# Optimization experiments

Hardware: AMD Instinct MI355X
Metric: run time of the kernel (lower is better)

Reference implementation:

```python
import jax, jax.numpy as jnp
import numpy as np

H, DM, DK, DV, DFF = 8, 512, 64, 64, 2048
B, S = 8, 1024
EPS = 1e-5


def layernorm_global(x):
    # torch nn.LayerNorm(x.size()[1:], elementwise_affine=False): normalize over ALL dims except batch
    mu = jnp.mean(x, axis=(1, 2), keepdims=True)
    var = jnp.var(x, axis=(1, 2), keepdims=True)
    return (x - mu) / jnp.sqrt(var + EPS)


def mha(q_in, k_in, v_in, wq, bq, wk, bk, wv, bv, wo, bo, causal):
    # wq/wk: [h, dk, dmodel], wv: [h, dv, dmodel] (torch Linear weight layout [out,in])
    q = jnp.einsum('bsd,hkd->bhsk', q_in, wq) + bq[None, :, None, :]
    k = jnp.einsum('bsd,hkd->bhsk', k_in, wk) + bk[None, :, None, :]
    v = jnp.einsum('bsd,hvd->bhsv', v_in, wv) + bv[None, :, None, :]
    scores = jnp.einsum('bhqk,bhsk->bhqs', q, k) / np.sqrt(DK).astype(np.float32)
    if causal:
        Sq = q_in.shape[1]
        mask = jnp.triu(jnp.full((Sq, Sq), -jnp.inf, dtype=scores.dtype), k=1)
        scores = scores + mask[None, None, :, :]
    w = jax.nn.softmax(scores, axis=-1)
    attn = jnp.einsum('bhqs,bhsv->bhqv', w, v)  # [b,h,q,dv]
    concat = attn.transpose(0, 2, 1, 3).reshape(q_in.shape[0], q_in.shape[1], H * DV)
    return concat @ wo.T + bo


def setup_inputs() -> dict:
    key = jax.random.key(0)
    ks = jax.random.split(key, 24)
    f = lambda k, shape: (jax.random.normal(k, shape, dtype=jnp.float32) * 0.02)
    inp = {
        'x_enc': jax.random.normal(ks[0], (B, S, DM), dtype=jnp.float32),
        'x_dec': jax.random.normal(ks[1], (B, S, DM), dtype=jnp.float32),
        # masked self-attention params
        'mq_w': f(ks[2], (H, DK, DM)), 'mq_b': f(ks[3], (H, DK)),
        'mk_w': f(ks[4], (H, DK, DM)), 'mk_b': f(ks[5], (H, DK)),
        'mv_w': f(ks[6], (H, DV, DM)), 'mv_b': f(ks[7], (H, DV)),
        'mo_w': f(ks[8], (DM, H * DV)), 'mo_b': f(ks[9], (DM,)),
        # cross-attention params
        'cq_w': f(ks[10], (H, DK, DM)), 'cq_b': f(ks[11], (H, DK)),
        'ck_w': f(ks[12], (H, DK, DM)), 'ck_b': f(ks[13], (H, DK)),
        'cv_w': f(ks[14], (H, DV, DM)), 'cv_b': f(ks[15], (H, DV)),
        'co_w': f(ks[16], (DM, H * DV)), 'co_b': f(ks[17], (DM,)),
        # feedforward params
        'f1_w': f(ks[18], (DFF, DM)), 'f1_b': f(ks[19], (DFF,)),
        'f2_w': f(ks[20], (DM, DFF)), 'f2_b': f(ks[21], (DM,)),
    }
    return inp


def reference(x_enc, x_dec,
              mq_w, mq_b, mk_w, mk_b, mv_w, mv_b, mo_w, mo_b,
              cq_w, cq_b, ck_w, ck_b, cv_w, cv_b, co_w, co_b,
              f1_w, f1_b, f2_w, f2_b):
    # masked self-attention block (dropout = identity at eval)
    x_dec_n = layernorm_global(x_dec)
    sa = mha(x_dec_n, x_dec_n, x_dec_n, mq_w, mq_b, mk_w, mk_b, mv_w, mv_b, mo_w, mo_b, causal=True)
    current = x_dec + sa
    # cross-attention block
    cur_n = layernorm_global(current)
    enc_n = layernorm_global(x_enc)
    ca = mha(cur_n, enc_n, enc_n, cq_w, cq_b, ck_w, ck_b, cv_w, cv_b, co_w, co_b, causal=False)
    result = current + ca
    # feedforward block
    res_n = layernorm_global(result)
    ff = jax.nn.relu(res_n @ f1_w.T + f1_b) @ f2_w.T + f2_b
    return result + ff
```

## Files before the change

kernel.cpp:

```cpp
#include <hip/hip_runtime.h>
#include <cmath>
#include <cstddef>
#include <cstdint>

#define BN   8
#define SN   1024
#define DMN  512
#define HN   8
#define DKN  64
#define DFFN 2048

typedef short           bf16x8   __attribute__((ext_vector_type(8)));
typedef float           f32x4    __attribute__((ext_vector_type(4)));
typedef float           f32x16   __attribute__((ext_vector_type(16)));
typedef unsigned short  ushortx4 __attribute__((ext_vector_type(4)));
typedef unsigned short  ushortx8 __attribute__((ext_vector_type(8)));
typedef unsigned int    uintx4   __attribute__((ext_vector_type(4)));
typedef unsigned short  u16;
typedef unsigned int    u32;

#define ATT_SC 0.18033688011112042f

__device__ __forceinline__ float bf2f(u16 u) {
  return __uint_as_float(((unsigned int)u) << 16);
}
__device__ __forceinline__ u16 f2bf(float f) {
  unsigned int u = __float_as_uint(f);
  u += 0x7FFFu + ((u >> 16) & 1u);
  return (u16)(u >> 16);
}
__device__ __forceinline__ u32 cvtpk_bf16(float lo, float hi) {
  u32 r;
  asm("v_cvt_pk_bf16_f32 %0, %1, %2" : "=v"(r) : "v"(lo), "v"(hi));
  return r;
}
__device__ __forceinline__ void gload_lds16(const u16* gsrc, u16* ldst) {
  __builtin_amdgcn_global_load_lds(
      (const __attribute__((address_space(1))) unsigned int*)gsrc,
      (__attribute__((address_space(3))) unsigned int*)ldst,
      16, 0, 0);
}
__device__ __forceinline__ int xcd_swz(int lid, int nwg) {
  const int cpx = nwg >> 3;
  return (lid & 7) * cpx + (lid >> 3);
}

__global__ __launch_bounds__(256) void cvt_weights(
    const float* p0, const float* p1, const float* p2, const float* p3,
    const float* p4, const float* p5, const float* p6, const float* p7,
    const float* p8, const float* p9, u16* __restrict__ dst) {
  const int gi = blockIdx.x * 256 + threadIdx.x;
  const int idx = gi * 4;
  const float* src; int off;
  if (idx < 2097152) {
    const int t = idx >> 18; off = idx & 262143;
    switch (t) {
      case 0: src = p0; break; case 1: src = p1; break;
      case 2: src = p2; break; case 3: src = p3; break;
      case 4: src = p4; break; case 5: src = p5; break;
      case 6: src = p6; break; default: src = p7; break;
    }
  } else if (idx < 3145728) { src = p8; off = idx - 2097152; }
  else                      { src = p9; off = idx - 3145728; }
  float4 v = *(const float4*)(src + off);
  ushortx4 o;
  o[0] = f2bf(v.x); o[1] = f2bf(v.y); o[2] = f2bf(v.z); o[3] = f2bf(v.w);
  *(ushortx4*)(dst + idx) = o;
}

__global__ __launch_bounds__(256) void pack_bias(const float* a, const float* b,
                                                 const float* c, const float* d,
                                                 const float* e, float* __restrict__ dst) {
  const int t = threadIdx.x;
#pragma unroll
  for (int i = t; i < 512; i += 256) {
    dst[i]        = a[i];
    dst[512 + i]  = b[i];
    dst[1024 + i] = c[i];
    dst[1536 + i] = d[i];
    dst[2048 + i] = e[i];
  }
}

__global__ __launch_bounds__(256) void ln_sum(const float* __restrict__ X,
                                              float2* __restrict__ part) {
  const int g = blockIdx.x, b = blockIdx.y, t = threadIdx.x;
  const float4* Xv = (const float4*)(X + (size_t)b * (SN * DMN) + (size_t)g * 8192);
  float s = 0.f, s2 = 0.f;
#pragma unroll
  for (int it = 0; it < 8; ++it) {
    float4 x = Xv[t + it * 256];
    s  += x.x + x.y + x.z + x.w;
    s2 += x.x*x.x + x.y*x.y + x.z*x.z + x.w*x.w;
  }
  __shared__ float rs[256], rq[256];
  rs[t] = s; rq[t] = s2;
  __syncthreads();
  for (int off = 128; off > 0; off >>= 1) {
    if (t < off) { rs[t] += rs[t + off]; rq[t] += rq[t + off]; }
    __syncthreads();
  }
  if (t == 0) part[b * 64 + g] = make_float2(rs[0], rq[0]);
}

__global__ __launch_bounds__(256) void ln_norm(const float* __restrict__ X,
                                               const float2* __restrict__ part,
                                               u16* __restrict__ Y) {
  const int g = blockIdx.x, b = blockIdx.y, t = threadIdx.x;
  __shared__ float ss[64], sq[64];
  if (t < 64) { float2 p = part[b * 64 + t]; ss[t] = p.x; sq[t] = p.y; }
  __syncthreads();
  float s = 0.f, q = 0.f;
#pragma unroll
  for (int j = 0; j < 64; ++j) { s += ss[j]; q += sq[j]; }
  const float inv_n = 1.f / (float)(SN * DMN);
  const float mu = s * inv_n;
  const float var = q * inv_n - mu * mu;
  const float rstd = rsqrtf(var + 1e-5f);
  const size_t base = (size_t)b * (SN * DMN) + (size_t)g * 8192;
  const float4* Xv = (const float4*)(X + base);
#pragma unroll
  for (int it = 0; it < 8; ++it) {
    float4 x = Xv[t + it * 256];
    ushortx4 o;
    o[0] = f2bf((x.x - mu) * rstd); o[1] = f2bf((x.y - mu) * rstd);
    o[2] = f2bf((x.z - mu) * rstd); o[3] = f2bf((x.w - mu) * rstd);
    *(ushortx4*)(Y + base + (size_t)(t + it * 256) * 4) = o;
  }
}

template<bool RELU, bool RES, int OMODE, int BM, bool QSC>
__global__ __launch_bounds__(256) void gemm_mfma(const u16* __restrict__ A,
                                                 const u16* __restrict__ W,
                                                 const float* __restrict__ bias,
                                                 const float* __restrict__ res,
                                                 void* __restrict__ Cv,
                                                 void* __restrict__ Cv2,
                                                 void* __restrict__ Cv3,
                                                 int M, int N, int K) {
  constexpr int MI = BM / 32;
  __shared__ u16 As[BM * 32];
  __shared__ u16 Bs[128 * 32];
  const int t = threadIdx.x;
  const int lane = t & 63, w = t >> 6;
  const int wm = w >> 1, wn = w & 1;

  const int gx = gridDim.x;
  const int lid = xcd_swz(blockIdx.y * gx + blockIdx.x, gx * gridDim.y);
  const int m0 = (lid / gx) * BM, n0 = (lid % gx) * 128;

  f32x4 acc[MI][4];
#pragma unroll
  for (int i = 0; i < MI; ++i)
#pragma unroll
    for (int j = 0; j < 4; ++j)
      acc[i][j] = (f32x4){0.f, 0.f, 0.f, 0.f};

  const int lrow = lane >> 2;
  const int lcol = (lane & 3) * 8;
  const int rofs = (lane & 15) * 32 + (lane >> 4) * 8;

  for (int k0 = 0; k0 < K; k0 += 32) {
    if (BM == 128) {
#pragma unroll
      for (int c = 0; c < 2; ++c) {
        const int r0 = w * 32 + c * 16;
        gload_lds16(A + (size_t)(m0 + r0 + lrow) * K + k0 + lcol, &As[r0 * 32]);
      }
    } else {
      const int r0 = w * 16;
      gload_lds16(A + (size_t)(m0 + r0 + lrow) * K + k0 + lcol, &As[r0 * 32]);
    }
#pragma unroll
    for (int c = 0; c < 2; ++c) {
      const int r0 = w * 32 + c * 16;
      gload_lds16(W + (size_t)(n0 + r0 + lrow) * K + k0 + lcol, &Bs[r0 * 32]);
    }
    __syncthreads();
    bf16x8 af[MI], bfr[4];
#pragma unroll
    for (int f = 0; f < MI; ++f)
      af[f]  = *(const bf16x8*)&As[(wm * (BM / 2) + f * 16) * 32 + rofs];
#pragma unroll
    for (int f = 0; f < 4; ++f)
      bfr[f] = *(const bf16x8*)&Bs[(wn * 64 + f * 16) * 32 + rofs];
#pragma unroll
    for (int i = 0; i < MI; ++i)
#pragma unroll
      for (int j = 0; j < 4; ++j)
        acc[i][j] = __builtin_amdgcn_mfma_f32_16x16x32_bf16(af[i], bfr[j], acc[i][j], 0, 0, 0);
    __syncthreads();
  }

  const int crow0 = (lane >> 4) * 4;
  const int ccol  = lane & 15;
  float bv[4];
#pragma unroll
  for (int j = 0; j < 4; ++j) bv[j] = bias[n0 + wn * 64 + j * 16 + ccol];

  u16* seg_out = nullptr;
  int  seg_n0 = 0;
  bool seg_vt = false;
  if (OMODE == 3) {
    if (n0 < 512)       { seg_out = (u16*)Cv;  seg_n0 = 0; }
    else if (n0 < 1024) { seg_out = (u16*)Cv2; seg_n0 = 512; }
    else                { seg_out = (u16*)Cv3; seg_n0 = 1024; seg_vt = true; }
  } else if (OMODE == 4) {
    if (n0 < 512)       { seg_out = (u16*)Cv;  seg_n0 = 0; }
    else                { seg_out = (u16*)Cv3; seg_n0 = 512; seg_vt = true; }
  }
  const bool do_scale = QSC && (OMODE != 3 || n0 < 512);

#pragma unroll
  for (int i = 0; i < MI; ++i) {
#pragma unroll
    for (int r = 0; r < 4; ++r) {
      const int m = m0 + wm * (BM / 2) + i * 16 + crow0 + r;
#pragma unroll
      for (int j = 0; j < 4; ++j) {
        const int n = n0 + wn * 64 + j * 16 + ccol;
        float v = acc[i][j][r] + bv[j];
        if (RELU) v = fmaxf(v, 0.f);
        if (RES)  v += res[(size_t)m * N + n];
        if (do_scale) v *= ATT_SC;
        if (OMODE == 0) {
          ((float*)Cv)[(size_t)m * N + n] = v;
        } else if (OMODE == 1) {
          ((u16*)Cv)[(size_t)m * N + n] = f2bf(v);
        } else {
          const int nn = n - seg_n0;
          if (!seg_vt) seg_out[(size_t)m * 512 + nn] = f2bf(v);
          else
            seg_out[(((size_t)(m >> 10) * HN + (nn >> 6)) * 64 + (nn & 63)) * SN + (m & 1023)] = f2bf(v);
        }
      }
    }
  }
}

#define QBLK 128
#define KVB  64

template<int CAUSAL, int NSPLIT>
__global__ __launch_bounds__(256) void attn_mfma(const u16* __restrict__ Q,
                                                 const u16* __restrict__ K,
                                                 const u16* __restrict__ VT,
                                                 u16* __restrict__ Out,
                                                 float* __restrict__ Lbuf) {
  const int lid = xcd_swz(blockIdx.y * 8 + blockIdx.x, 512);
  const int qb = lid & 7;
  const int bh = lid >> 3;
  const int sp = (NSPLIT > 1) ? blockIdx.z : 0;
  const int b = bh >> 3, h = bh & 7;
  const int t = threadIdx.x;
  const int lane = t & 63, w = t >> 6;
  const int l31 = lane & 31, hi = lane >> 5;

  __shared__ __align__(16) u16 Ks[64 * 64];
  __shared__ __align__(16) u16 Vts[8 * 512];

  const int qw0 = qb * QBLK + w * 32;
  const int qglob = qw0 + l31;

  bf16x8 bq[4];
#pragma unroll
  for (int dk = 0; dk < 4; ++dk)
    bq[dk] = *(const bf16x8*)(Q + (size_t)(b * SN + qglob) * 512
                                + h * 64 + dk * 16 + hi * 8);

  f32x16 acc0 = {}, acc1 = {};
  float l_run = 0.f;

  const int ntile = CAUSAL ? (2 * qb + 2) : (SN / KVB);
  const int n4 = (ntile + NSPLIT - 1) / NSPLIT;
  const int kt0 = sp * n4;
  const int ktend = (kt0 + n4 < ntile) ? (kt0 + n4) : ntile;

  const int srow = t >> 2;
  const int ss0  = 2 * (t & 3);
  const u16* kg0 = K + (size_t)(b * SN + srow) * 512 + h * 64 + ((ss0 ^ (srow & 7)) * 8);
  const u16* kg1 = K + (size_t)(b * SN + srow) * 512 + h * 64 + (((ss0 + 1) ^ (srow & 7)) * 8);
  u16* kd0 = &Ks[t * 16];
  u16* kd1 = &Ks[t * 16 + 8];
  const int vd = t & 63, vp = t >> 6;
  const u16* vg = VT + ((size_t)bh * 64 + vd) * SN + vp * 16;
  u16* vdst0 = &Vts[(2 * vp) * 512 + vd * 8];
  u16* vdst1 = &Vts[(2 * vp + 1) * 512 + vd * 8];

  ushortx8 kr0, kr1, vr0, vr1;
  {
    const size_t ka = (size_t)kt0 * KVB * 512;
    kr0 = *(const ushortx8*)(kg0 + ka);
    kr1 = *(const ushortx8*)(kg1 + ka);
    vr0 = *(const ushortx8*)(vg + kt0 * KVB);
    vr1 = *(const ushortx8*)(vg + kt0 * KVB + 8);
  }

  for (int kt = kt0; kt < ktend; ++kt) {
    const int k0 = kt * KVB;
    __syncthreads();
    *(ushortx8*)kd0 = kr0;
    *(ushortx8*)kd1 = kr1;
    *(ushortx8*)vdst0 = vr0;
    *(ushortx8*)vdst1 = vr1;
    if (kt + 1 < ktend) {
      const size_t kadv = (size_t)(kt + 1) * KVB * 512;
      kr0 = *(const ushortx8*)(kg0 + kadv);
      kr1 = *(const ushortx8*)(kg1 + kadv);
      vr0 = *(const ushortx8*)(vg + (kt + 1) * KVB);
      vr1 = *(const ushortx8*)(vg + (kt + 1) * KVB + 8);
    }
    __syncthreads();

    if (CAUSAL && k0 > qw0 + 31) continue;

    f32x16 s0 = {}, s1 = {};
    __builtin_amdgcn_s_setprio(1);
#pragma unroll
    for (int dk = 0; dk < 4; ++dk) {
      const int boff = dk * 32 + hi * 16;
      const int sw = boff ^ ((l31 & 7) << 4);
      bf16x8 a0 = *(const bf16x8*)&Ks[l31 * 64 + (sw >> 1)];
      bf16x8 a1 = *(const bf16x8*)&Ks[(32 + l31) * 64 + (sw >> 1)];
      s0 = __builtin_amdgcn_mfma_f32_32x32x16_bf16(a0, bq[dk], s0, 0, 0, 0);
      s1 = __builtin_amdgcn_mfma_f32_32x32x16_bf16(a1, bq[dk], s1, 0, 0, 0);
    }
    __builtin_amdgcn_s_setprio(0);

    if (CAUSAL && (k0 + KVB - 1 > qw0)) {
#pragma unroll
      for (int i = 0; i < 16; ++i) {
        const int krow = (i & 3) + 8 * (i >> 2) + 4 * hi;
        if (k0 + krow > qglob)      s0[i] = -INFINITY;
        if (k0 + 32 + krow > qglob) s1[i] = -INFINITY;
      }
    }
    float ps = 0.f;
#pragma unroll
    for (int i = 0; i < 16; ++i) {
      s0[i] = exp2f(s0[i]); ps += s0[i];
      s1[i] = exp2f(s1[i]); ps += s1[i];
    }
    l_run += ps;

    __builtin_amdgcn_s_setprio(1);
#pragma unroll
    for (int ksb = 0; ksb < 4; ++ksb) {
      const int kb = ksb & 1;
      u32 A0, A1, B0, B1;
      if (ksb < 2) {
        A0 = cvtpk_bf16(s0[8*kb + 0], s0[8*kb + 1]);
        A1 = cvtpk_bf16(s0[8*kb + 2], s0[8*kb + 3]);
        B0 = cvtpk_bf16(s0[8*kb + 4], s0[8*kb + 5]);
        B1 = cvtpk_bf16(s0[8*kb + 6], s0[8*kb + 7]);
      } else {
        A0 = cvtpk_bf16(s1[8*kb + 0], s1[8*kb + 1]);
        A1 = cvtpk_bf16(s1[8*kb + 2], s1[8*kb + 3]);
        B0 = cvtpk_bf16(s1[8*kb + 4], s1[8*kb + 5]);
        B1 = cvtpk_bf16(s1[8*kb + 6], s1[8*kb + 7]);
      }
      const u32 xA0 = __shfl_xor(A0, 32), xA1 = __shfl_xor(A1, 32);
      const u32 xB0 = __shfl_xor(B0, 32), xB1 = __shfl_xor(B1, 32);
      uintx4 pw;
      pw[0] = hi ? xB0 : A0;
      pw[1] = hi ? xB1 : A1;
      pw[2] = hi ? B0 : xA0;
      pw[3] = hi ? B1 : xA1;
      const bf16x8 pb = *(const bf16x8*)&pw;
      const bf16x8 av0 = *(const bf16x8*)&Vts[(ksb * 2 + hi) * 512 + l31 * 8];
      const bf16x8 av1 = *(const bf16x8*)&Vts[(ksb * 2 + hi) * 512 + (32 + l31) * 8];
      acc0 = __builtin_amdgcn_mfma_f32_32x32x16_bf16(av0, pb, acc0, 0, 0, 0);
      acc1 = __builtin_amdgcn_mfma_f32_32x32x16_bf16(av1, pb, acc1, 0, 0, 0);
    }
    __builtin_amdgcn_s_setprio(0);
  }

  l_run += __shfl_xor(l_run, 32);
  if (NSPLIT == 1) {
    const float inv = 1.f / l_run;
    u16* op = Out + (size_t)(b * SN + qglob) * 512 + h * 64;
#pragma unroll
    for (int g = 0; g < 4; ++g) {
      ushortx4 o0, o1;
#pragma unroll
      for (int r = 0; r < 4; ++r) {
        o0[r] = f2bf(acc0[4*g + r] * inv);
        o1[r] = f2bf(acc1[4*g + r] * inv);
      }
      *(ushortx4*)(op + 4*hi + 8*g)      = o0;
      *(ushortx4*)(op + 32 + 4*hi + 8*g) = o1;
    }
  } else {
    u16* op = Out + (((size_t)(sp * 64 + bh)) * 1024 + qglob) * 64;
#pragma unroll
    for (int g = 0; g < 4; ++g) {
      ushortx4 o0, o1;
#pragma unroll
      for (int r = 0; r < 4; ++r) {
        o0[r] = f2bf(acc0[4*g + r]);
        o1[r] = f2bf(acc1[4*g + r]);
      }
      *(ushortx4*)(op + 4*hi + 8*g)      = o0;
      *(ushortx4*)(op + 32 + 4*hi + 8*g) = o1;
    }
    if (hi == 0)
      Lbuf[((size_t)(sp * 64 + bh)) * 1024 + qglob] = l_run;
  }
}

__global__ __launch_bounds__(256) void attn_merge2(const u16* __restrict__ Pacc,
                                                   const float* __restrict__ Lbuf,
                                                   u16* __restrict__ O) {
  const int tid = blockIdx.x * 256 + threadIdx.x;
  const int qh = tid >> 3;
  const int d0 = (tid & 7) * 8;
  const int bh = qh >> 10, q = qh & 1023;
  const int b = bh >> 3, h = bh & 7;

  const float l = Lbuf[(size_t)bh * 1024 + q] + Lbuf[(size_t)(64 + bh) * 1024 + q];
  const float inv = 1.f / l;
  ushortx8 a0 = *(const ushortx8*)(Pacc + ((size_t)bh * 1024 + q) * 64 + d0);
  ushortx8 a1 = *(const ushortx8*)(Pacc + ((size_t)(64 + bh) * 1024 + q) * 64 + d0);
  ushortx8 ov;
#pragma unroll
  for (int e = 0; e < 8; ++e)
    ov[e] = f2bf((bf2f(a0[e]) + bf2f(a1[e])) * inv);
  *(ushortx8*)(O + ((size_t)(b * 1024 + q) * 512) + h * 64 + d0) = ov;
}

extern "C" void kernel_launch(void* const* d_in, const int* in_sizes, int n_in,
                              void* d_out, int out_size, void* d_ws, size_t ws_size,
                              hipStream_t stream) {
  const float* x_enc = (const float*)d_in[0];
  const float* x_dec = (const float*)d_in[1];
  const float* mq_w = (const float*)d_in[2];  const float* mq_b = (const float*)d_in[3];
  const float* mk_w = (const float*)d_in[4];  const float* mk_b = (const float*)d_in[5];
  const float* mv_w = (const float*)d_in[6];  const float* mv_b = (const float*)d_in[7];
  const float* mo_w = (const float*)d_in[8];  const float* mo_b = (const float*)d_in[9];
  const float* cq_w = (const float*)d_in[10]; const float* cq_b = (const float*)d_in[11];
  const float* ck_w = (const float*)d_in[12]; const float* ck_b = (const float*)d_in[13];
  const float* cv_w = (const float*)d_in[14]; const float* cv_b = (const float*)d_in[15];
  const float* co_w = (const float*)d_in[16]; const float* co_b = (const float*)d_in[17];
  const float* f1_w = (const float*)d_in[18]; const float* f1_b = (const float*)d_in[19];
  const float* f2_w = (const float*)d_in[20]; const float* f2_b = (const float*)d_in[21];
  float* out = (float*)d_out;

  char* wsb = (char*)d_ws;
  float* o5  = (float*)(wsb + 0);
  float* o6  = (float*)(wsb + (16u << 20));
  u16* Qb    = (u16*)(wsb + (32u << 20));
  u16* Kb    = (u16*)(wsb + (40u << 20));
  u16* VTb   = (u16*)(wsb + (48u << 20));
  u16* B0    = (u16*)(wsb + (56u << 20));
  u16* B1    = (u16*)(wsb + (64u << 20));
  u16* FF1   = (u16*)(wsb + (72u << 20));
  u16* WB    = (u16*)(wsb + (104u << 20));
  float2* part = (float2*)(wsb + (112u << 20));
  float* BC  = (float*)(wsb + (113u << 20));

  u16* Pacc   = FF1;
  float* Lbuf = (float*)B1;

  u16* wb_mq = WB + 0 * 262144;
  u16* wb_mo = WB + 3 * 262144;
  u16* wb_cq = WB + 4 * 262144;
  u16* wb_ck = WB + 5 * 262144;
  u16* wb_co = WB + 7 * 262144;
  u16* wb_f1 = WB + 8 * 262144; u16* wb_f2 = WB + 8 * 262144 + 1048576;

  const int M = BN * SN;
  dim3 ln_grid(64, BN);
  dim3 g512s(512 / 128, M / 64);
  dim3 g1024(1024 / 128, M / 128);
  dim3 g1536(1536 / 128, M / 128);
  dim3 g2048(2048 / 128, M / 128);
  dim3 attn_grid_c(SN / QBLK, BN * HN, 2);
  dim3 attn_grid_x(SN / QBLK, BN * HN, 1);

  cvt_weights<<<4096, 256, 0, stream>>>(mq_w, mk_w, mv_w, mo_w, cq_w, ck_w, cv_w, co_w,
                                        f1_w, f2_w, WB);
  pack_bias<<<1, 256, 0, stream>>>(mq_b, mk_b, mv_b, ck_b, cv_b, BC);

  ln_sum<<<ln_grid, 256, 0, stream>>>(x_dec, part);
  ln_norm<<<ln_grid, 256, 0, stream>>>(x_dec, part, B0);
  gemm_mfma<false, false, 3, 128, true><<<g1536, 256, 0, stream>>>(B0, wb_mq, BC, nullptr,
                                                                   Qb, Kb, VTb, M, 1536, 512);
  attn_mfma<1, 2><<<attn_grid_c, 256, 0, stream>>>(Qb, Kb, VTb, Pacc, Lbuf);
  attn_merge2<<<2048, 256, 0, stream>>>(Pacc, Lbuf, B0);
  gemm_mfma<false, true, 0, 64, false><<<g512s, 256, 0, stream>>>(B0, wb_mo, mo_b, x_dec,
                                                                  o5, nullptr, nullptr, M, 512, 512);

  ln_sum<<<ln_grid, 256, 0, stream>>>(o5, part);
  ln_norm<<<ln_grid, 256, 0, stream>>>(o5, part, B0);
  ln_sum<<<ln_grid, 256, 0, stream>>>(x_enc, part);
  ln_norm<<<ln_grid, 256, 0, stream>>>(x_enc, part, B1);
  gemm_mfma<false, false, 1, 64, true><<<g512s, 256, 0, stream>>>(B0, wb_cq, cq_b, nullptr,
                                                                  Qb, nullptr, nullptr, M, 512, 512);
  gemm_mfma<false, false, 4, 128, false><<<g1024, 256, 0, stream>>>(B1, wb_ck, BC + 1536, nullptr,
                                                                    Kb, nullptr, VTb, M, 1024, 512);
  attn_mfma<0, 1><<<attn_grid_x, 256, 0, stream>>>(Qb, Kb, VTb, B0, nullptr);
  gemm_mfma<false, true, 0, 64, false><<<g512s, 256, 0, stream>>>(B0, wb_co, co_b, o5,
                                                                  o6, nullptr, nullptr, M, 512, 512);

  ln_sum<<<ln_grid, 256, 0, stream>>>(o6, part);
  ln_norm<<<ln_grid, 256, 0, stream>>>(o6, part, B0);
  gemm_mfma<true, false, 1, 128, false><<<g2048, 256, 0, stream>>>(B0, wb_f1, f1_b, nullptr,
                                                                   FF1, nullptr, nullptr, M, 2048, 512);
  gemm_mfma<false, true, 0, 64, false><<<g512s, 256, 0, stream>>>(FF1, wb_f2, f2_b, o6,
                                                                  out, nullptr, nullptr, M, 512, 2048);
}
```

Before: 279.3 us.

## Store residual stream in bf16 and split cross-attention over KV halves

The intermediate residual tensors o5 and o6 are now stored as bf16 instead of fp32. The layernorm kernels and the residual-add GEMM epilogues gain bf16-input variants so they read half the bytes. Cross-attention now always uses the two-way KV split with a merge kernel, which gives it more parallel blocks at the cost of an extra merge pass. Keeping the residual in bf16 loses precision in the accumulated residual stream.

Result: slower. 286.9 us (+2.7%).

```diff
diff --git a/kernel.cpp b/kernel.cpp
--- a/kernel.cpp
+++ b/kernel.cpp
@@ -82,16 +82,27 @@
   }
 }
 
-__global__ __launch_bounds__(256) void ln_sum(const float* __restrict__ X,
+template<bool INBF>
+__global__ __launch_bounds__(256) void ln_sum(const void* __restrict__ Xv_,
                                               float2* __restrict__ part) {
   const int g = blockIdx.x, b = blockIdx.y, t = threadIdx.x;
-  const float4* Xv = (const float4*)(X + (size_t)b * (SN * DMN) + (size_t)g * 8192);
   float s = 0.f, s2 = 0.f;
-#pragma unroll
-  for (int it = 0; it < 8; ++it) {
-    float4 x = Xv[t + it * 256];
-    s  += x.x + x.y + x.z + x.w;
-    s2 += x.x*x.x + x.y*x.y + x.z*x.z + x.w*x.w;
+  if (INBF) {
+    const ushortx8* Xv = (const ushortx8*)((const u16*)Xv_ + (size_t)b * (SN * DMN) + (size_t)g * 8192);
+#pragma unroll
+    for (int it = 0; it < 4; ++it) {
+      ushortx8 x = Xv[t + it * 256];
+#pragma unroll
+      for (int e = 0; e < 8; ++e) { float f = bf2f(x[e]); s += f; s2 += f * f; }
+    }
+  } else {
+    const float4* Xv = (const float4*)((const float*)Xv_ + (size_t)b * (SN * DMN) + (size_t)g * 8192);
+#pragma unroll
+    for (int it = 0; it < 8; ++it) {
+      float4 x = Xv[t + it * 256];
+      s  += x.x + x.y + x.z + x.w;
+      s2 += x.x*x.x + x.y*x.y + x.z*x.z + x.w*x.w;
+    }
   }
   __shared__ float rs[256], rq[256];
   rs[t] = s; rq[t] = s2;
@@ -103,7 +114,8 @@
   if (t == 0) part[b * 64 + g] = make_float2(rs[0], rq[0]);
 }
 
-__global__ __launch_bounds__(256) void ln_norm(const float* __restrict__ X,
+template<bool INBF>
+__global__ __launch_bounds__(256) void ln_norm(const void* __restrict__ Xv_,
                                                const float2* __restrict__ part,
                                                u16* __restrict__ Y) {
   const int g = blockIdx.x, b = blockIdx.y, t = threadIdx.x;
@@ -118,22 +130,34 @@
   const float var = q * inv_n - mu * mu;
   const float rstd = rsqrtf(var + 1e-5f);
   const size_t base = (size_t)b * (SN * DMN) + (size_t)g * 8192;
-  const float4* Xv = (const float4*)(X + base);
-#pragma unroll
-  for (int it = 0; it < 8; ++it) {
-    float4 x = Xv[t + it * 256];
-    ushortx4 o;
-    o[0] = f2bf((x.x - mu) * rstd); o[1] = f2bf((x.y - mu) * rstd);
-    o[2] = f2bf((x.z - mu) * rstd); o[3] = f2bf((x.w - mu) * rstd);
-    *(ushortx4*)(Y + base + (size_t)(t + it * 256) * 4) = o;
-  }
-}
-
-template<bool RELU, bool RES, int OMODE, int BM, bool QSC>
+  if (INBF) {
+    const ushortx8* Xv = (const ushortx8*)((const u16*)Xv_ + base);
+#pragma unroll
+    for (int it = 0; it < 4; ++it) {
+      ushortx8 x = Xv[t + it * 256];
+      ushortx8 o;
+#pragma unroll
+      for (int e = 0; e < 8; ++e) o[e] = f2bf((bf2f(x[e]) - mu) * rstd);
+      *(ushortx8*)(Y + base + (size_t)(t + it * 256) * 8) = o;
+    }
+  } else {
+    const float4* Xv = (const float4*)((const float*)Xv_ + base);
+#pragma unroll
+    for (int it = 0; it < 8; ++it) {
+      float4 x = Xv[t + it * 256];
+      ushortx4 o;
+      o[0] = f2bf((x.x - mu) * rstd); o[1] = f2bf((x.y - mu) * rstd);
+      o[2] = f2bf((x.z - mu) * rstd); o[3] = f2bf((x.w - mu) * rstd);
+      *(ushortx4*)(Y + base + (size_t)(t + it * 256) * 4) = o;
+    }
+  }
+}
+
+template<bool RELU, bool RES, bool RESBF, int OMODE, int BM, bool QSC>
 __global__ __launch_bounds__(256) void gemm_mfma(const u16* __restrict__ A,
                                                  const u16* __restrict__ W,
                                                  const float* __restrict__ bias,
-                                                 const float* __restrict__ res,
+                                                 const void* __restrict__ resv,
                                                  void* __restrict__ Cv,
                                                  void* __restrict__ Cv2,
                                                  void* __restrict__ Cv3,
@@ -221,7 +245,10 @@
         const int n = n0 + wn * 64 + j * 16 + ccol;
         float v = acc[i][j][r] + bv[j];
         if (RELU) v = fmaxf(v, 0.f);
-        if (RES)  v += res[(size_t)m * N + n];
+        if (RES) {
+          if (RESBF) v += bf2f(((const u16*)resv)[(size_t)m * N + n]);
+          else       v += ((const float*)resv)[(size_t)m * N + n];
+        }
         if (do_scale) v *= ATT_SC;
         if (OMODE == 0) {
           ((float*)Cv)[(size_t)m * N + n] = v;
@@ -376,36 +403,20 @@
   }
 
   l_run += __shfl_xor(l_run, 32);
-  if (NSPLIT == 1) {
-    const float inv = 1.f / l_run;
-    u16* op = Out + (size_t)(b * SN + qglob) * 512 + h * 64;
-#pragma unroll
-    for (int g = 0; g < 4; ++g) {
-      ushortx4 o0, o1;
-#pragma unroll
-      for (int r = 0; r < 4; ++r) {
-        o0[r] = f2bf(acc0[4*g + r] * inv);
-        o1[r] = f2bf(acc1[4*g + r] * inv);
-      }
-      *(ushortx4*)(op + 4*hi + 8*g)      = o0;
-      *(ushortx4*)(op + 32 + 4*hi + 8*g) = o1;
-    }
-  } else {
-    u16* op = Out + (((size_t)(sp * 64 + bh)) * 1024 + qglob) * 64;
-#pragma unroll
-    for (int g = 0; g < 4; ++g) {
-      ushortx4 o0, o1;
-#pragma unroll
-      for (int r = 0; r < 4; ++r) {
-        o0[r] = f2bf(acc0[4*g + r]);
-        o1[r] = f2bf(acc1[4*g + r]);
-      }
-      *(ushortx4*)(op + 4*hi + 8*g)      = o0;
-      *(ushortx4*)(op + 32 + 4*hi + 8*g) = o1;
-    }
-    if (hi == 0)
-      Lbuf[((size_t)(sp * 64 + bh)) * 1024 + qglob] = l_run;
-  }
+  u16* op = Out + (((size_t)(sp * 64 + bh)) * 1024 + qglob) * 64;
+#pragma unroll
+  for (int g = 0; g < 4; ++g) {
+    ushortx4 o0, o1;
+#pragma unroll
+    for (int r = 0; r < 4; ++r) {
+      o0[r] = f2bf(acc0[4*g + r]);
+      o1[r] = f2bf(acc1[4*g + r]);
+    }
+    *(ushortx4*)(op + 4*hi + 8*g)      = o0;
+    *(ushortx4*)(op + 32 + 4*hi + 8*g) = o1;
+  }
+  if (hi == 0)
+    Lbuf[((size_t)(sp * 64 + bh)) * 1024 + qglob] = l_run;
 }
 
 __global__ __launch_bounds__(256) void attn_merge2(const u16* __restrict__ Pacc,
@@ -446,8 +457,8 @@
   float* out = (float*)d_out;
 
   char* wsb = (char*)d_ws;
-  float* o5  = (float*)(wsb + 0);
-  float* o6  = (float*)(wsb + (16u << 20));
+  u16* o5    = (u16*)(wsb + 0);
+  u16* o6    = (u16*)(wsb + (16u << 20));
   u16* Qb    = (u16*)(wsb + (32u << 20));
   u16* Kb    = (u16*)(wsb + (40u << 20));
   u16* VTb   = (u16*)(wsb + (48u << 20));
@@ -474,38 +485,38 @@
   dim3 g1024(1024 / 128, M / 128);
   dim3 g1536(1536 / 128, M / 128);
   dim3 g2048(2048 / 128, M / 128);
-  dim3 attn_grid_c(SN / QBLK, BN * HN, 2);
-  dim3 attn_grid_x(SN / QBLK, BN * HN, 1);
+  dim3 attn_grid(SN / QBLK, BN * HN, 2);
 
   cvt_weights<<<4096, 256, 0, stream>>>(mq_w, mk_w, mv_w, mo_w, cq_w, ck_w, cv_w, co_w,
                                         f1_w, f2_w, WB);
   pack_bias<<<1, 256, 0, stream>>>(mq_b, mk_b, mv_b, ck_b, cv_b, BC);
 
-  ln_sum<<<ln_grid, 256, 0, stream>>>(x_dec, part);
-  ln_norm<<<ln_grid, 256, 0, stream>>>(x_dec, part, B0);
-  gemm_mfma<false, false, 3, 128, true><<<g1536, 256, 0, stream>>>(B0, wb_mq, BC, nullptr,
-                                                                   Qb, Kb, VTb, M, 1536, 512);
-  attn_mfma<1, 2><<<attn_grid_c, 256, 0, stream>>>(Qb, Kb, VTb, Pacc, Lbuf);
+  ln_sum<false><<<ln_grid, 256, 0, stream>>>(x_dec, part);
+  ln_norm<false><<<ln_grid, 256, 0, stream>>>(x_dec, part, B0);
+  gemm_mfma<false, false, false, 3, 128, true><<<g1536, 256, 0, stream>>>(B0, wb_mq, BC, nullptr,
+                                                                          Qb, Kb, VTb, M, 1536, 512);
+  attn_mfma<1, 2><<<attn_grid, 256, 0, stream>>>(Qb, Kb, VTb, Pacc, Lbuf);
   attn_merge2<<<2048, 256, 0, stream>>>(Pacc, Lbuf, B0);
-  gemm_mfma<false, true, 0, 64, false><<<g512s, 256, 0, stream>>>(B0, wb_mo, mo_b, x_dec,
-                                                                  o5, nullptr, nullptr, M, 512, 512);
-
-  ln_sum<<<ln_grid, 256, 0, stream>>>(o5, part);
-  ln_norm<<<ln_grid, 256, 0, stream>>>(o5, part, B0);
-  ln_sum<<<ln_grid, 256, 0, stream>>>(x_enc, part);
-  ln_norm<<<ln_grid, 256, 0, stream>>>(x_enc, part, B1);
-  gemm_mfma<false, false, 1, 64, true><<<g512s, 256, 0, stream>>>(B0, wb_cq, cq_b, nullptr,
-                                                                  Qb, nullptr, nullptr, M, 512, 512);
-  gemm_mfma<false, false, 4, 128, false><<<g1024, 256, 0, stream>>>(B1, wb_ck, BC + 1536, nullptr,
-                                                                    Kb, nullptr, VTb, M, 1024, 512);
-  attn_mfma<0, 1><<<attn_grid_x, 256, 0, stream>>>(Qb, Kb, VTb, B0, nullptr);
-  gemm_mfma<false, true, 0, 64, false><<<g512s, 256, 0, stream>>>(B0, wb_co, co_b, o5,
-                                                                  o6, nullptr, nullptr, M, 512, 512);
-
-  ln_sum<<<ln_grid, 256, 0, stream>>>(o6, part);
-  ln_norm<<<ln_grid, 256, 0, stream>>>(o6, part, B0);
-  gemm_mfma<true, false, 1, 128, false><<<g2048, 256, 0, stream>>>(B0, wb_f1, f1_b, nullptr,
-                                                                   FF1, nullptr, nullptr, M, 2048, 512);
-  gemm_mfma<false, true, 0, 64, false><<<g512s, 256, 0, stream>>>(FF1, wb_f2, f2_b, o6,
-                                                                  out, nullptr, nullptr, M, 512, 2048);
-}
+  gemm_mfma<false, true, false, 1, 64, false><<<g512s, 256, 0, stream>>>(B0, wb_mo, mo_b, x_dec,
+                                                                         o5, nullptr, nullptr, M, 512, 512);
+
+  ln_sum<true><<<ln_grid, 256, 0, stream>>>(o5, part);
+  ln_norm<true><<<ln_grid, 256, 0, stream>>>(o5, part, B0);
+  ln_sum<false><<<ln_grid, 256, 0, stream>>>(x_enc, part);
+  ln_norm<false><<<ln_grid, 256, 0, stream>>>(x_enc, part, B1);
+  gemm_mfma<false, false, false, 1, 64, true><<<g512s, 256, 0, stream>>>(B0, wb_cq, cq_b, nullptr,
+                                                                         Qb, nullptr, nullptr, M, 512, 512);
+  gemm_mfma<false, false, false, 4, 128, false><<<g1024, 256, 0, stream>>>(B1, wb_ck, BC + 1536, nullptr,
+                                                                           Kb, nullptr, VTb, M, 1024, 512);
+  attn_mfma<0, 2><<<attn_grid, 256, 0, stream>>>(Qb, Kb, VTb, Pacc, Lbuf);
+  attn_merge2<<<2048, 256, 0, stream>>>(Pacc, Lbuf, B0);
+  gemm_mfma<false, true, true, 1, 64, false><<<g512s, 256, 0, stream>>>(B0, wb_co, co_b, o5,
+                                                                        o6, nullptr, nullptr, M, 512, 512);
+
+  ln_sum<true><<<ln_grid, 256, 0, stream>>>(o6, part);
+  ln_norm<true><<<ln_grid, 256, 0, stream>>>(o6, part, B0);
+  gemm_mfma<true, false, false, 1, 128, false><<<g2048, 256, 0, stream>>>(B0, wb_f1, f1_b, nullptr,
+                                                                          FF1, nullptr, nullptr, M, 2048, 512);
+  gemm_mfma<false, true, true, 0, 64, false><<<g512s, 256, 0, stream>>>(FF1, wb_f2, f2_b, o6,
+                                                                        out, nullptr, nullptr, M, 512, 2048);
+}
```
